# Optimization experiments

Measured on AMD Instinct MI355X. Metric: run time of the kernel, lower is better.

The kernel has to match this reference:

```python
import jax, jax.numpy as jnp
import numpy as np

N = 50000       # nodes
E = 1600000     # edges (avg degree 32)
DIN = 128
DOUT = 128
EPS = 1e-5      # torch BatchNorm1d default eps


def setup_inputs() -> dict:
    key = jax.random.key(0)
    ks = jax.random.split(key, 6)
    x = jax.random.normal(ks[0], (N, DIN), dtype=jnp.float32)
    edge_index = jax.random.randint(ks[1], (2, E), 0, N, dtype=jnp.int32)
    edge_weight = jax.random.uniform(ks[2], (E,), dtype=jnp.float32)
    stdv = 1.0 / float(np.sqrt(DOUT))
    # main linear: uniform(-stdv, stdv) per reset_parameters
    W = jax.random.uniform(ks[3], (DOUT, DIN), dtype=jnp.float32, minval=-stdv, maxval=stdv)
    b = jnp.zeros((DOUT,), jnp.float32)
    # residual linear
    Wres = jax.random.uniform(ks[4], (DOUT, DIN), dtype=jnp.float32, minval=-stdv, maxval=stdv)
    bres = jnp.zeros((DOUT,), jnp.float32)
    # batchnorm affine params
    gamma = jnp.ones((DOUT,), jnp.float32)
    beta = jnp.zeros((DOUT,), jnp.float32)
    return {"x": x, "edge_index": edge_index, "edge_weight": edge_weight,
            "W": W, "b": b, "Wres": Wres, "bres": bres,
            "gamma": gamma, "beta": beta}


def reference(x, edge_index, edge_weight, W, b, Wres, bres, gamma, beta):
    # support = self.linear(x)
    support = x @ W.T + b                                   # [N, DOUT]
    # out = spmm(graph, support): out[d] = sum_e w_e * support[src_e] for dst_e == d
    src, dst = edge_index[0], edge_index[1]
    msgs = support[src] * edge_weight[:, None]              # [E, DOUT] gather
    out = jax.ops.segment_sum(msgs, dst, num_segments=N)    # [N, DOUT] scatter-add
    # batchnorm (training-mode batch statistics, biased variance)
    mean = jnp.mean(out, axis=0)
    var = jnp.var(out, axis=0)
    out = (out - mean) * jax.lax.rsqrt(var + EPS) * gamma + beta
    # relu
    out = jax.nn.relu(out)
    # residual projection of the input
    out = out + x @ Wres.T + bres
    return out
```

## Files before the change

### kernel.cpp

```cpp
#include <hip/hip_runtime.h>

#define DF 128
#define BN_EPS 1e-5f

typedef short s16x8 __attribute__((ext_vector_type(8)));
typedef float f32x4 __attribute__((ext_vector_type(4)));

__device__ __forceinline__ ushort f2b(float f) {
    uint u = __float_as_uint(f);
    u += 0x7fffu + ((u >> 16) & 1u);
    return (ushort)(u >> 16);
}
__device__ __forceinline__ float b2f_lo(uint v) { return __uint_as_float(v << 16); }
__device__ __forceinline__ float b2f_hi(uint v) { return __uint_as_float(v & 0xffff0000u); }

__global__ __launch_bounds__(256) void cvt_f32_bf16(
    const float* __restrict__ in, ushort* __restrict__ out, long n4)
{
    long t = (long)blockIdx.x * 256 + threadIdx.x;
    if (t >= n4) return;
    float4 v = reinterpret_cast<const float4*>(in)[t];
    ushort4 o;
    o.x = f2b(v.x); o.y = f2b(v.y); o.z = f2b(v.z); o.w = f2b(v.w);
    reinterpret_cast<ushort4*>(out)[t] = o;
}

__global__ __launch_bounds__(256) void gemm_mfma(
    const float* __restrict__ x, const ushort* __restrict__ Wcat,
    const float* __restrict__ b, const float* __restrict__ bres,
    ushort* __restrict__ support, float* __restrict__ res, int N)
{
    const int wave = threadIdx.x >> 6;
    const int lane = threadIdx.x & 63;
    const int r0   = (blockIdx.x * 4 + wave) * 16;
    if (r0 >= N) return;
    const int lrow = lane & 15;
    const int g4   = lane >> 4;
    const int koff = g4 * 8;
    const int row  = r0 + lrow;
    const bool rok = row < N;
    const int  ar  = rok ? row : (N - 1);

    s16x8 xf[4];
#pragma unroll
    for (int kb = 0; kb < 4; ++kb) {
        float4 f0 = reinterpret_cast<const float4*>(x)[(size_t)ar * 32 + kb * 8 + g4 * 2];
        float4 f1 = reinterpret_cast<const float4*>(x)[(size_t)ar * 32 + kb * 8 + g4 * 2 + 1];
        s16x8 v;
        v[0] = (short)f2b(f0.x); v[1] = (short)f2b(f0.y);
        v[2] = (short)f2b(f0.z); v[3] = (short)f2b(f0.w);
        v[4] = (short)f2b(f1.x); v[5] = (short)f2b(f1.y);
        v[6] = (short)f2b(f1.z); v[7] = (short)f2b(f1.w);
        xf[kb] = v;
    }

#pragma unroll
    for (int ct = 0; ct < 16; ++ct) {
        f32x4 acc = {0.f, 0.f, 0.f, 0.f};
#pragma unroll
        for (int kb = 0; kb < 4; ++kb) {
            s16x8 wf = *reinterpret_cast<const s16x8*>(
                &Wcat[(size_t)(ct * 16 + lrow) * 128 + kb * 32 + koff]);
            acc = __builtin_amdgcn_mfma_f32_16x16x32_bf16(wf, xf[kb], acc, 0, 0, 0);
        }
        if (rok) {
            int c0 = ct * 16 + 4 * g4;
            if (ct < 8) {
                float4 bias = *reinterpret_cast<const float4*>(&b[c0]);
                ushort4 o;
                o.x = f2b(acc[0] + bias.x); o.y = f2b(acc[1] + bias.y);
                o.z = f2b(acc[2] + bias.z); o.w = f2b(acc[3] + bias.w);
                *reinterpret_cast<ushort4*>(&support[(size_t)row * 128 + c0]) = o;
            } else {
                int c = c0 - 128;
                float4 bias = *reinterpret_cast<const float4*>(&bres[c]);
                float4 o = make_float4(acc[0] + bias.x, acc[1] + bias.y,
                                       acc[2] + bias.z, acc[3] + bias.w);
                *reinterpret_cast<float4*>(&res[(size_t)row * 128 + c]) = o;
            }
        }
    }
}

__global__ __launch_bounds__(512) void bin_count(
    const int* __restrict__ dst, int* __restrict__ bktcnt, int E)
{
    __shared__ int h[1024];
    const int tid = threadIdx.x;
    for (int i = tid; i < 1024; i += 512) h[i] = 0;
    __syncthreads();
    const int base = blockIdx.x * 4096;
#pragma unroll
    for (int k = 0; k < 8; ++k) {
        int i = base + k * 512 + tid;
        if (i < E) atomicAdd(&h[dst[i] >> 6], 1);
    }
    __syncthreads();
    for (int i = tid; i < 1024; i += 512)
        if (h[i]) atomicAdd(&bktcnt[i], h[i]);
}

__global__ __launch_bounds__(512) void bin_scan(
    const int* __restrict__ bktcnt, int* __restrict__ bktptr,
    int* __restrict__ bktcur, int NBKT, int E)
{
    __shared__ int s[1024];
    const int t = threadIdx.x;
    int v0 = (t < NBKT) ? bktcnt[t] : 0;
    int v1 = (t + 512 < NBKT) ? bktcnt[t + 512] : 0;
    s[t] = v0; s[t + 512] = v1;
    __syncthreads();
    for (int off = 1; off < 1024; off <<= 1) {
        int a0 = (t >= off) ? s[t - off] : 0;
        int a1 = (t + 512 >= off) ? s[t + 512 - off] : 0;
        __syncthreads();
        s[t] += a0; s[t + 512] += a1;
        __syncthreads();
    }
    if (t < NBKT)       { int e = s[t] - v0;       bktptr[t] = e;       bktcur[t] = e; }
    if (t + 512 < NBKT) { int e = s[t+512] - v1;   bktptr[t+512] = e;   bktcur[t+512] = e; }
    if (t == 0) bktptr[NBKT] = E;
}

__global__ __launch_bounds__(512) void bin_scatter(
    const int* __restrict__ src, const int* __restrict__ dst,
    const float* __restrict__ ew, int* __restrict__ bktcur,
    uint2* __restrict__ recs, int E)
{
    __shared__ int cntl[1024];
    __shared__ int scn[1024];
    __shared__ int lcur[1024];
    __shared__ int gbase[1024];
    __shared__ uint2 stage[4096];
    const int tid = threadIdx.x;
    for (int i = tid; i < 1024; i += 512) cntl[i] = 0;
    __syncthreads();
    const int base = blockIdx.x * 4096;
    int myd[8];
#pragma unroll
    for (int k = 0; k < 8; ++k) {
        int i = base + k * 512 + tid;
        myd[k] = (i < E) ? dst[i] : -1;
        if (myd[k] >= 0) atomicAdd(&cntl[myd[k] >> 6], 1);
    }
    __syncthreads();
#pragma unroll
    for (int j = 0; j < 2; ++j) scn[tid + j * 512] = cntl[tid + j * 512];
    __syncthreads();
    for (int off = 1; off < 1024; off <<= 1) {
        int a[2];
#pragma unroll
        for (int j = 0; j < 2; ++j) {
            int idx = tid + j * 512;
            a[j] = (idx >= off) ? scn[idx - off] : 0;
        }
        __syncthreads();
#pragma unroll
        for (int j = 0; j < 2; ++j) scn[tid + j * 512] += a[j];
        __syncthreads();
    }
#pragma unroll
    for (int j = 0; j < 2; ++j) {
        int idx = tid + j * 512;
        int ex = scn[idx] - cntl[idx];
        scn[idx] = ex;
        lcur[idx] = ex;
    }
    for (int i = tid; i < 1024; i += 512) {
        int c = cntl[i];
        gbase[i] = c ? atomicAdd(&bktcur[i], c) : 0;
    }
    __syncthreads();
#pragma unroll
    for (int k = 0; k < 8; ++k) {
        int i = base + k * 512 + tid;
        if (i < E) {
            int d = myd[k];
            int bb = d >> 6;
            int p = atomicAdd(&lcur[bb], 1);
            uint w0 = (uint)src[i] | ((uint)(d & 63) << 16) | ((uint)bb << 22);
            stage[p] = make_uint2(w0, __float_as_uint(ew[i]));
        }
    }
    __syncthreads();
    const int nloc = min(4096, E - base);
    for (int j = tid; j < nloc; j += 512) {
        uint2 r = stage[j];
        int bb = r.x >> 22;
        int pos = gbase[bb] + (j - scn[bb]);
        recs[pos] = make_uint2(r.x & 0x3fffffu, r.y);
    }
}

__global__ __launch_bounds__(512) void spmm_sorted(
    const ushort* __restrict__ supportb, const uint2* __restrict__ recs,
    const int* __restrict__ bktptr, float* __restrict__ agg,
    float* __restrict__ bnacc, int N)
{
    __shared__ uint2 sorted[2048];
    __shared__ int hcnt[32];
    __shared__ int hoff[32];
    __shared__ int hcur[32];

    const int tid  = threadIdx.x;
    const int wv   = tid >> 6;
    const int lane = tid & 63;
    const int b    = blockIdx.x >> 1;
    const int half = blockIdx.x & 1;
    const int beg  = bktptr[b], end = bktptr[b + 1];
    const uint* sup = reinterpret_cast<const uint*>(supportb);

    float ax[4], ay[4];
#pragma unroll
    for (int r = 0; r < 4; ++r) { ax[r] = 0.f; ay[r] = 0.f; }

    for (int cbeg = beg; cbeg < end; cbeg += 2048) {
        const int cn = min(2048, end - cbeg);
        if (tid < 32) hcnt[tid] = 0;
        __syncthreads();
        uint2 myr[4];
        bool  mv[4];
#pragma unroll
        for (int u = 0; u < 4; ++u) {
            int j = tid + u * 512;
            mv[u] = false;
            if (j < cn) {
                myr[u] = recs[cbeg + j];
                int dl = (myr[u].x >> 16) & 63;
                if ((dl >> 5) == half) {
                    mv[u] = true;
                    atomicAdd(&hcnt[dl & 31], 1);
                }
            }
        }
        __syncthreads();
        if (tid < 32) {
            int v = hcnt[tid];
            int inc = v;
#pragma unroll
            for (int off = 1; off < 32; off <<= 1) {
                int t = __shfl_up(inc, off, 32);
                if (tid >= off) inc += t;
            }
            hoff[tid] = inc - v;
            hcur[tid] = inc - v;
        }
        __syncthreads();
#pragma unroll
        for (int u = 0; u < 4; ++u) {
            if (mv[u]) {
                int r = (myr[u].x >> 16) & 31;
                int p = atomicAdd(&hcur[r], 1);
                sorted[p] = myr[u];
            }
        }
        __syncthreads();
#pragma unroll
        for (int rr = 0; rr < 4; ++rr) {
            const int r  = wv * 4 + rr;
            const int s0 = hoff[r];
            const int s1 = s0 + hcnt[r];
            int k = s0;
            for (; k + 4 <= s1; k += 4) {
                uint2 e0 = sorted[k], e1 = sorted[k+1], e2 = sorted[k+2], e3 = sorted[k+3];
                uint v0 = sup[(size_t)(e0.x & 0xffffu) * 64 + lane];
                uint v1 = sup[(size_t)(e1.x & 0xffffu) * 64 + lane];
                uint v2 = sup[(size_t)(e2.x & 0xffffu) * 64 + lane];
                uint v3 = sup[(size_t)(e3.x & 0xffffu) * 64 + lane];
                float w0 = __uint_as_float(e0.y), w1 = __uint_as_float(e1.y);
                float w2 = __uint_as_float(e2.y), w3 = __uint_as_float(e3.y);
                ax[rr] = fmaf(b2f_lo(v0), w0, ax[rr]); ay[rr] = fmaf(b2f_hi(v0), w0, ay[rr]);
                ax[rr] = fmaf(b2f_lo(v1), w1, ax[rr]); ay[rr] = fmaf(b2f_hi(v1), w1, ay[rr]);
                ax[rr] = fmaf(b2f_lo(v2), w2, ax[rr]); ay[rr] = fmaf(b2f_hi(v2), w2, ay[rr]);
                ax[rr] = fmaf(b2f_lo(v3), w3, ax[rr]); ay[rr] = fmaf(b2f_hi(v3), w3, ay[rr]);
            }
            for (; k < s1; ++k) {
                uint2 e = sorted[k];
                uint v = sup[(size_t)(e.x & 0xffffu) * 64 + lane];
                float w = __uint_as_float(e.y);
                ax[rr] = fmaf(b2f_lo(v), w, ax[rr]);
                ay[rr] = fmaf(b2f_hi(v), w, ay[rr]);
            }
        }
        __syncthreads();
    }

    const int row0 = b * 64 + half * 32 + wv * 4;
#pragma unroll
    for (int rr = 0; rr < 4; ++rr) {
        int gr = row0 + rr;
        if (gr < N)
            reinterpret_cast<float2*>(agg)[(size_t)gr * 64 + lane] = make_float2(ax[rr], ay[rr]);
    }

    float s1x = 0.f, s1y = 0.f, s2x = 0.f, s2y = 0.f;
#pragma unroll
    for (int rr = 0; rr < 4; ++rr) {
        s1x += ax[rr]; s1y += ay[rr];
        s2x = fmaf(ax[rr], ax[rr], s2x);
        s2y = fmaf(ay[rr], ay[rr], s2y);
    }
    float* red = reinterpret_cast<float*>(sorted);
    red[wv * 256 + 2 * lane]            = s1x;
    red[wv * 256 + 2 * lane + 1]        = s1y;
    red[2048 + wv * 256 + 2 * lane]     = s2x;
    red[2048 + wv * 256 + 2 * lane + 1] = s2y;
    __syncthreads();
    if (tid < 128) {
        float t1 = 0.f, t2 = 0.f;
#pragma unroll
        for (int w8 = 0; w8 < 8; ++w8) {
            t1 += red[w8 * 256 + tid];
            t2 += red[2048 + w8 * 256 + tid];
        }
        unsafeAtomicAdd(&bnacc[tid], t1);
        unsafeAtomicAdd(&bnacc[128 + tid], t2);
    }
}

__global__ void bn_finalize(const float* __restrict__ bnacc,
                            const float* __restrict__ gamma,
                            const float* __restrict__ beta,
                            float* __restrict__ scsh, float invN)
{
    int j = threadIdx.x;
    float mean = bnacc[j] * invN;
    float var  = bnacc[128 + j] * invN - mean * mean;
    float sc   = gamma[j] * rsqrtf(var + BN_EPS);
    scsh[j]       = sc;
    scsh[128 + j] = beta[j] - mean * sc;
}

__global__ __launch_bounds__(256) void bn_apply(
    const float* __restrict__ agg, const float* __restrict__ scsh,
    float* __restrict__ out, long total4)
{
    long t = (long)blockIdx.x * 256 + threadIdx.x;
    if (t >= total4) return;
    int f4 = (int)(t & 31);
    float4 v  = reinterpret_cast<const float4*>(agg)[t];
    float4 sc = reinterpret_cast<const float4*>(scsh)[f4];
    float4 sh = reinterpret_cast<const float4*>(scsh)[32 + f4];
    float4 r  = reinterpret_cast<float4*>(out)[t];
    float4 o;
    o.x = fmaxf(fmaf(v.x, sc.x, sh.x), 0.f) + r.x;
    o.y = fmaxf(fmaf(v.y, sc.y, sh.y), 0.f) + r.y;
    o.z = fmaxf(fmaf(v.z, sc.z, sh.z), 0.f) + r.z;
    o.w = fmaxf(fmaf(v.w, sc.w, sh.w), 0.f) + r.w;
    reinterpret_cast<float4*>(out)[t] = o;
}

extern "C" void kernel_launch(void* const* d_in, const int* in_sizes, int n_in,
                              void* d_out, int out_size, void* d_ws, size_t ws_size,
                              hipStream_t stream)
{
    const float* x     = (const float*)d_in[0];
    const int*   ei    = (const int*)  d_in[1];
    const float* ew    = (const float*)d_in[2];
    const float* W     = (const float*)d_in[3];
    const float* b     = (const float*)d_in[4];
    const float* Wres  = (const float*)d_in[5];
    const float* bres  = (const float*)d_in[6];
    const float* gamma = (const float*)d_in[7];
    const float* beta  = (const float*)d_in[8];

    const int N = in_sizes[0] / DF;
    const int E = in_sizes[2];
    const int* srci = ei;
    const int* dsti = ei + E;
    const int NBKT = (N + 63) >> 6;

    float*  fws      = (float*)d_ws;
    float*  agg      = fws;
    float*  bnacc    = agg + (size_t)N * DF;
    int*    bktcnt   = (int*)(bnacc + 256);
    int*    bktptr   = bktcnt + 1056;
    int*    bktcur   = bktptr + 1056;
    float*  scsh     = (float*)(bktcur + 1056);
    ushort* supportb = (ushort*)(scsh + 256);
    uint2*  recs     = (uint2*)(supportb + (size_t)N * DF);
    ushort* Wcat     = (ushort*)(recs + (size_t)E);
    float*  out      = (float*)d_out;

    hipMemsetAsync(bnacc, 0, (256 + 1056) * sizeof(float), stream);

    cvt_f32_bf16<<<16, 256, 0, stream>>>(W,    Wcat,            4096);
    cvt_f32_bf16<<<16, 256, 0, stream>>>(Wres, Wcat + 128 * DF, 4096);

    gemm_mfma<<<(N + 63) / 64, 256, 0, stream>>>(x, Wcat, b, bres, supportb, out, N);

    const int eb = (E + 4095) / 4096;
    bin_count<<<eb, 512, 0, stream>>>(dsti, bktcnt, E);
    bin_scan<<<1, 512, 0, stream>>>(bktcnt, bktptr, bktcur, NBKT, E);
    bin_scatter<<<eb, 512, 0, stream>>>(srci, dsti, ew, bktcur, recs, E);

    spmm_sorted<<<NBKT * 2, 512, 0, stream>>>(supportb, recs, bktptr, agg, bnacc, N);

    bn_finalize<<<1, 128, 0, stream>>>(bnacc, gamma, beta, scsh, 1.0f / (float)N);

    long t4 = (long)N * (DF / 4);
    bn_apply<<<(int)((t4 + 255) / 256), 256, 0, stream>>>(agg, scsh, out, t4);
}
```

Baseline: 262.4 us.

## Merge small kernels, widen GEMM rows per wave, unroll SpMM gather by eight

Merges the two weight-conversion launches into one and folds the BN finalize step into bn_apply, so each block recomputes scale and shift into shared memory. The GEMM wave now handles 32 rows with two accumulators, reusing each W fragment twice. bin_count reads dst with int4 loads, and bin_scatter uses half-size chunks so more blocks run with less shared memory each. The SpMM inner loop gains an 8-way unrolled gather to keep more loads in flight. Costs are higher register pressure in the GEMM and SpMM kernels and redundant finalize work in every bn_apply block.

```diff
diff --git a/kernel.cpp b/kernel.cpp
--- a/kernel.cpp
+++ b/kernel.cpp
@@ -14,15 +14,18 @@
 __device__ __forceinline__ float b2f_lo(uint v) { return __uint_as_float(v << 16); }
 __device__ __forceinline__ float b2f_hi(uint v) { return __uint_as_float(v & 0xffff0000u); }
 
-__global__ __launch_bounds__(256) void cvt_f32_bf16(
-    const float* __restrict__ in, ushort* __restrict__ out, long n4)
-{
-    long t = (long)blockIdx.x * 256 + threadIdx.x;
-    if (t >= n4) return;
-    float4 v = reinterpret_cast<const float4*>(in)[t];
+__global__ __launch_bounds__(256) void cvt_weights(
+    const float* __restrict__ W, const float* __restrict__ Wres,
+    ushort* __restrict__ Wcat)
+{
+    const int half = blockIdx.x >> 4;
+    const float* src = half ? Wres : W;
+    ushort* dstp = Wcat + half * 128 * DF;
+    int t = (blockIdx.x & 15) * 256 + threadIdx.x;
+    float4 v = reinterpret_cast<const float4*>(src)[t];
     ushort4 o;
     o.x = f2b(v.x); o.y = f2b(v.y); o.z = f2b(v.z); o.w = f2b(v.w);
-    reinterpret_cast<ushort4*>(out)[t] = o;
+    reinterpret_cast<ushort4*>(dstp)[t] = o;
 }
 
 __global__ __launch_bounds__(256) void gemm_mfma(
@@ -32,51 +35,76 @@
 {
     const int wave = threadIdx.x >> 6;
     const int lane = threadIdx.x & 63;
-    const int r0   = (blockIdx.x * 4 + wave) * 16;
-    if (r0 >= N) return;
+    const int base = (blockIdx.x * 4 + wave) * 32;
+    if (base >= N) return;
     const int lrow = lane & 15;
     const int g4   = lane >> 4;
     const int koff = g4 * 8;
-    const int row  = r0 + lrow;
-    const bool rok = row < N;
-    const int  ar  = rok ? row : (N - 1);
-
-    s16x8 xf[4];
+    const int row0 = base + lrow;
+    const int row1 = base + 16 + lrow;
+    const bool ok0 = row0 < N, ok1 = row1 < N;
+    const int  a0r = ok0 ? row0 : (N - 1);
+    const int  a1r = ok1 ? row1 : (N - 1);
+
+    s16x8 xf0[4], xf1[4];
 #pragma unroll
     for (int kb = 0; kb < 4; ++kb) {
-        float4 f0 = reinterpret_cast<const float4*>(x)[(size_t)ar * 32 + kb * 8 + g4 * 2];
-        float4 f1 = reinterpret_cast<const float4*>(x)[(size_t)ar * 32 + kb * 8 + g4 * 2 + 1];
+        float4 f0 = reinterpret_cast<const float4*>(x)[(size_t)a0r * 32 + kb * 8 + g4 * 2];
+        float4 f1 = reinterpret_cast<const float4*>(x)[(size_t)a0r * 32 + kb * 8 + g4 * 2 + 1];
         s16x8 v;
         v[0] = (short)f2b(f0.x); v[1] = (short)f2b(f0.y);
         v[2] = (short)f2b(f0.z); v[3] = (short)f2b(f0.w);
         v[4] = (short)f2b(f1.x); v[5] = (short)f2b(f1.y);
         v[6] = (short)f2b(f1.z); v[7] = (short)f2b(f1.w);
-        xf[kb] = v;
+        xf0[kb] = v;
+        float4 g0 = reinterpret_cast<const float4*>(x)[(size_t)a1r * 32 + kb * 8 + g4 * 2];
+        float4 g1 = reinterpret_cast<const float4*>(x)[(size_t)a1r * 32 + kb * 8 + g4 * 2 + 1];
+        s16x8 w;
+        w[0] = (short)f2b(g0.x); w[1] = (short)f2b(g0.y);
+        w[2] = (short)f2b(g0.z); w[3] = (short)f2b(g0.w);
+        w[4] = (short)f2b(g1.x); w[5] = (short)f2b(g1.y);
+        w[6] = (short)f2b(g1.z); w[7] = (short)f2b(g1.w);
+        xf1[kb] = w;
     }
 
 #pragma unroll
     for (int ct = 0; ct < 16; ++ct) {
-        f32x4 acc = {0.f, 0.f, 0.f, 0.f};
+        f32x4 acc0 = {0.f, 0.f, 0.f, 0.f};
+        f32x4 acc1 = {0.f, 0.f, 0.f, 0.f};
 #pragma unroll
         for (int kb = 0; kb < 4; ++kb) {
             s16x8 wf = *reinterpret_cast<const s16x8*>(
                 &Wcat[(size_t)(ct * 16 + lrow) * 128 + kb * 32 + koff]);
-            acc = __builtin_amdgcn_mfma_f32_16x16x32_bf16(wf, xf[kb], acc, 0, 0, 0);
-        }
-        if (rok) {
-            int c0 = ct * 16 + 4 * g4;
-            if (ct < 8) {
-                float4 bias = *reinterpret_cast<const float4*>(&b[c0]);
+            acc0 = __builtin_amdgcn_mfma_f32_16x16x32_bf16(wf, xf0[kb], acc0, 0, 0, 0);
+            acc1 = __builtin_amdgcn_mfma_f32_16x16x32_bf16(wf, xf1[kb], acc1, 0, 0, 0);
+        }
+        int c0 = ct * 16 + 4 * g4;
+        if (ct < 8) {
+            float4 bias = *reinterpret_cast<const float4*>(&b[c0]);
+            if (ok0) {
                 ushort4 o;
-                o.x = f2b(acc[0] + bias.x); o.y = f2b(acc[1] + bias.y);
-                o.z = f2b(acc[2] + bias.z); o.w = f2b(acc[3] + bias.w);
-                *reinterpret_cast<ushort4*>(&support[(size_t)row * 128 + c0]) = o;
-            } else {
-                int c = c0 - 128;
-                float4 bias = *reinterpret_cast<const float4*>(&bres[c]);
-                float4 o = make_float4(acc[0] + bias.x, acc[1] + bias.y,
-                                       acc[2] + bias.z, acc[3] + bias.w);
-                *reinterpret_cast<float4*>(&res[(size_t)row * 128 + c]) = o;
+                o.x = f2b(acc0[0] + bias.x); o.y = f2b(acc0[1] + bias.y);
+                o.z = f2b(acc0[2] + bias.z); o.w = f2b(acc0[3] + bias.w);
+                *reinterpret_cast<ushort4*>(&support[(size_t)row0 * 128 + c0]) = o;
+            }
+            if (ok1) {
+                ushort4 o;
+                o.x = f2b(acc1[0] + bias.x); o.y = f2b(acc1[1] + bias.y);
+                o.z = f2b(acc1[2] + bias.z); o.w = f2b(acc1[3] + bias.w);
+                *reinterpret_cast<ushort4*>(&support[(size_t)row1 * 128 + c0]) = o;
+            }
+        } else {
+            int c = c0 - 128;
+            float4 bias = *reinterpret_cast<const float4*>(&bres[c]);
+            if (ok0) {
+                float4 o = make_float4(acc0[0] + bias.x, acc0[1] + bias.y,
+                                       acc0[2] + bias.z, acc0[3] + bias.w);
+                *reinterpret_cast<float4*>(&res[(size_t)row0 * 128 + c]) = o;
+            }
+            if (ok1) {
+                float4 o = make_float4(acc1[0] + bias.x, acc1[1] + bias.y,
+                                       acc1[2] + bias.z, acc1[3] + bias.w);
+                *reinterpret_cast<float4*>(&res[(size_t)row1 * 128 + c]) = o;
             }
         }
     }
@@ -91,9 +119,18 @@
     __syncthreads();
     const int base = blockIdx.x * 4096;
 #pragma unroll
-    for (int k = 0; k < 8; ++k) {
-        int i = base + k * 512 + tid;
-        if (i < E) atomicAdd(&h[dst[i] >> 6], 1);
+    for (int k = 0; k < 2; ++k) {
+        int i = base + k * 2048 + tid * 4;
+        if (i + 3 < E) {
+            int4 d = *reinterpret_cast<const int4*>(&dst[i]);
+            atomicAdd(&h[d.x >> 6], 1);
+            atomicAdd(&h[d.y >> 6], 1);
+            atomicAdd(&h[d.z >> 6], 1);
+            atomicAdd(&h[d.w >> 6], 1);
+        } else {
+            for (int j = 0; j < 4; ++j)
+                if (i + j < E) atomicAdd(&h[dst[i + j] >> 6], 1);
+        }
     }
     __syncthreads();
     for (int i = tid; i < 1024; i += 512)
@@ -131,14 +168,14 @@
     __shared__ int scn[1024];
     __shared__ int lcur[1024];
     __shared__ int gbase[1024];
-    __shared__ uint2 stage[4096];
+    __shared__ uint2 stage[2048];
     const int tid = threadIdx.x;
     for (int i = tid; i < 1024; i += 512) cntl[i] = 0;
     __syncthreads();
-    const int base = blockIdx.x * 4096;
-    int myd[8];
-#pragma unroll
-    for (int k = 0; k < 8; ++k) {
+    const int base = blockIdx.x * 2048;
+    int myd[4];
+#pragma unroll
+    for (int k = 0; k < 4; ++k) {
         int i = base + k * 512 + tid;
         myd[k] = (i < E) ? dst[i] : -1;
         if (myd[k] >= 0) atomicAdd(&cntl[myd[k] >> 6], 1);
@@ -172,7 +209,7 @@
     }
     __syncthreads();
 #pragma unroll
-    for (int k = 0; k < 8; ++k) {
+    for (int k = 0; k < 4; ++k) {
         int i = base + k * 512 + tid;
         if (i < E) {
             int d = myd[k];
@@ -183,7 +220,7 @@
         }
     }
     __syncthreads();
-    const int nloc = min(4096, E - base);
+    const int nloc = min(2048, E - base);
     for (int j = tid; j < nloc; j += 512) {
         uint2 r = stage[j];
         int bb = r.x >> 22;
@@ -261,6 +298,30 @@
             const int s0 = hoff[r];
             const int s1 = s0 + hcnt[r];
             int k = s0;
+            for (; k + 8 <= s1; k += 8) {
+                uint2 e0 = sorted[k],   e1 = sorted[k+1], e2 = sorted[k+2], e3 = sorted[k+3];
+                uint2 e4 = sorted[k+4], e5 = sorted[k+5], e6 = sorted[k+6], e7 = sorted[k+7];
+                uint v0 = sup[(size_t)(e0.x & 0xffffu) * 64 + lane];
+                uint v1 = sup[(size_t)(e1.x & 0xffffu) * 64 + lane];
+                uint v2 = sup[(size_t)(e2.x & 0xffffu) * 64 + lane];
+                uint v3 = sup[(size_t)(e3.x & 0xffffu) * 64 + lane];
+                uint v4 = sup[(size_t)(e4.x & 0xffffu) * 64 + lane];
+                uint v5 = sup[(size_t)(e5.x & 0xffffu) * 64 + lane];
+                uint v6 = sup[(size_t)(e6.x & 0xffffu) * 64 + lane];
+                uint v7 = sup[(size_t)(e7.x & 0xffffu) * 64 + lane];
+                float w0 = __uint_as_float(e0.y), w1 = __uint_as_float(e1.y);
+                float w2 = __uint_as_float(e2.y), w3 = __uint_as_float(e3.y);
+                float w4 = __uint_as_float(e4.y), w5 = __uint_as_float(e5.y);
+                float w6 = __uint_as_float(e6.y), w7 = __uint_as_float(e7.y);
+                ax[rr] = fmaf(b2f_lo(v0), w0, ax[rr]); ay[rr] = fmaf(b2f_hi(v0), w0, ay[rr]);
+                ax[rr] = fmaf(b2f_lo(v1), w1, ax[rr]); ay[rr] = fmaf(b2f_hi(v1), w1, ay[rr]);
+                ax[rr] = fmaf(b2f_lo(v2), w2, ax[rr]); ay[rr] = fmaf(b2f_hi(v2), w2, ay[rr]);
+                ax[rr] = fmaf(b2f_lo(v3), w3, ax[rr]); ay[rr] = fmaf(b2f_hi(v3), w3, ay[rr]);
+                ax[rr] = fmaf(b2f_lo(v4), w4, ax[rr]); ay[rr] = fmaf(b2f_hi(v4), w4, ay[rr]);
+                ax[rr] = fmaf(b2f_lo(v5), w5, ax[rr]); ay[rr] = fmaf(b2f_hi(v5), w5, ay[rr]);
+                ax[rr] = fmaf(b2f_lo(v6), w6, ax[rr]); ay[rr] = fmaf(b2f_hi(v6), w6, ay[rr]);
+                ax[rr] = fmaf(b2f_lo(v7), w7, ax[rr]); ay[rr] = fmaf(b2f_hi(v7), w7, ay[rr]);
+            }
             for (; k + 4 <= s1; k += 4) {
                 uint2 e0 = sorted[k], e1 = sorted[k+1], e2 = sorted[k+2], e3 = sorted[k+3];
                 uint v0 = sup[(size_t)(e0.x & 0xffffu) * 64 + lane];
@@ -318,29 +379,27 @@
     }
 }
 
-__global__ void bn_finalize(const float* __restrict__ bnacc,
-                            const float* __restrict__ gamma,
-                            const float* __restrict__ beta,
-                            float* __restrict__ scsh, float invN)
-{
-    int j = threadIdx.x;
-    float mean = bnacc[j] * invN;
-    float var  = bnacc[128 + j] * invN - mean * mean;
-    float sc   = gamma[j] * rsqrtf(var + BN_EPS);
-    scsh[j]       = sc;
-    scsh[128 + j] = beta[j] - mean * sc;
-}
-
 __global__ __launch_bounds__(256) void bn_apply(
-    const float* __restrict__ agg, const float* __restrict__ scsh,
-    float* __restrict__ out, long total4)
-{
-    long t = (long)blockIdx.x * 256 + threadIdx.x;
+    const float* __restrict__ agg, const float* __restrict__ bnacc,
+    const float* __restrict__ gamma, const float* __restrict__ beta,
+    float* __restrict__ out, float invN, long total4)
+{
+    __shared__ float s_sc[128], s_sh[128];
+    const int tid = threadIdx.x;
+    if (tid < 128) {
+        float mean = bnacc[tid] * invN;
+        float var  = bnacc[128 + tid] * invN - mean * mean;
+        float sc   = gamma[tid] * rsqrtf(var + BN_EPS);
+        s_sc[tid] = sc;
+        s_sh[tid] = beta[tid] - mean * sc;
+    }
+    __syncthreads();
+    long t = (long)blockIdx.x * 256 + tid;
     if (t >= total4) return;
     int f4 = (int)(t & 31);
     float4 v  = reinterpret_cast<const float4*>(agg)[t];
-    float4 sc = reinterpret_cast<const float4*>(scsh)[f4];
-    float4 sh = reinterpret_cast<const float4*>(scsh)[32 + f4];
+    float4 sc = reinterpret_cast<const float4*>(s_sc)[f4];
+    float4 sh = reinterpret_cast<const float4*>(s_sh)[f4];
     float4 r  = reinterpret_cast<float4*>(out)[t];
     float4 o;
     o.x = fmaxf(fmaf(v.x, sc.x, sh.x), 0.f) + r.x;
@@ -376,28 +435,24 @@
     int*    bktcnt   = (int*)(bnacc + 256);
     int*    bktptr   = bktcnt + 1056;
     int*    bktcur   = bktptr + 1056;
-    float*  scsh     = (float*)(bktcur + 1056);
-    ushort* supportb = (ushort*)(scsh + 256);
+    ushort* supportb = (ushort*)(bktcur + 1056);
     uint2*  recs     = (uint2*)(supportb + (size_t)N * DF);
     ushort* Wcat     = (ushort*)(recs + (size_t)E);
     float*  out      = (float*)d_out;
 
     hipMemsetAsync(bnacc, 0, (256 + 1056) * sizeof(float), stream);
 
-    cvt_f32_bf16<<<16, 256, 0, stream>>>(W,    Wcat,            4096);
-    cvt_f32_bf16<<<16, 256, 0, stream>>>(Wres, Wcat + 128 * DF, 4096);
-
-    gemm_mfma<<<(N + 63) / 64, 256, 0, stream>>>(x, Wcat, b, bres, supportb, out, N);
-
-    const int eb = (E + 4095) / 4096;
-    bin_count<<<eb, 512, 0, stream>>>(dsti, bktcnt, E);
+    cvt_weights<<<32, 256, 0, stream>>>(W, Wres, Wcat);
+
+    gemm_mfma<<<(N + 127) / 128, 256, 0, stream>>>(x, Wcat, b, bres, supportb, out, N);
+
+    bin_count<<<(E + 4095) / 4096, 512, 0, stream>>>(dsti, bktcnt, E);
     bin_scan<<<1, 512, 0, stream>>>(bktcnt, bktptr, bktcur, NBKT, E);
-    bin_scatter<<<eb, 512, 0, stream>>>(srci, dsti, ew, bktcur, recs, E);
+    bin_scatter<<<(E + 2047) / 2048, 512, 0, stream>>>(srci, dsti, ew, bktcur, recs, E);
 
     spmm_sorted<<<NBKT * 2, 512, 0, stream>>>(supportb, recs, bktptr, agg, bnacc, N);
 
-    bn_finalize<<<1, 128, 0, stream>>>(bnacc, gamma, beta, scsh, 1.0f / (float)N);
-
     long t4 = (long)N * (DF / 4);
-    bn_apply<<<(int)((t4 + 255) / 256), 256, 0, stream>>>(agg, scsh, out, t4);
-}
+    bn_apply<<<(int)((t4 + 255) / 256), 256, 0, stream>>>(
+        agg, bnacc, gamma, beta, out, 1.0f / (float)N, t4);
+}
```

After: 252.6 us. 3.8% less time.
